# Kernel tuning notes

Hardware: AMD Instinct MI355X
Metric: run time of the kernel (lower is better)

The kernel has to match this reference:

```python
import jax, jax.numpy as jnp
import numpy as np
import math

N_HEAD = 16
HEAD_DIM = 64
BASE = 10000.0

def setup_inputs() -> dict:
    key = jax.random.key(0)
    k1, k2, k3, k4 = jax.random.split(key, 4)
    B, T, C = 2, 2048, 1024
    x = jax.random.normal(k1, (B, T, C), dtype=jnp.float32)
    w_attn = jax.random.normal(k2, (3 * C, C), dtype=jnp.float32) * 0.02
    w_proj = jax.random.normal(k3, (C, C), dtype=jnp.float32) * 0.02
    delta = jax.random.normal(k4, (N_HEAD, HEAD_DIM), dtype=jnp.float32) * 0.5
    return {"x": x, "w_attn": w_attn, "w_proj": w_proj, "delta": delta}

def reference(x, w_attn, w_proj, delta):
    B, T, C = x.shape
    H, D = N_HEAD, HEAD_DIM
    # qkv projection (nn.Linear, no bias): x @ W^T
    qkv = jnp.einsum('btc,ec->bte', x, w_attn)
    q, k, v = jnp.split(qkv, 3, axis=-1)
    q = q.reshape(B, T, H, D).transpose(0, 2, 1, 3)  # (B,H,T,D)
    k = k.reshape(B, T, H, D).transpose(0, 2, 1, 3)
    v = v.reshape(B, T, H, D).transpose(0, 2, 1, 3)
    # PoPE: d frequencies per head
    inv_freq = 1.0 / (BASE ** (jnp.arange(D, dtype=jnp.float32) / D))  # (D,)
    t = jnp.arange(T, dtype=jnp.float32)
    freqs = t[:, None] * inv_freq[None, :]            # (T,D)
    cos_pos = jnp.cos(freqs)[None, None]              # (1,1,T,D)
    sin_pos = jnp.sin(freqs)[None, None]
    mu_q = jax.nn.softplus(q)
    mu_k = jax.nn.softplus(k)
    d = jnp.clip(delta, -2.0 * math.pi, 0.0)          # (H,D)
    cos_d = jnp.cos(d)[None, :, None, :]              # (1,H,1,D)
    sin_d = jnp.sin(d)[None, :, None, :]
    q_real = mu_q * cos_pos
    q_imag = mu_q * sin_pos
    k_real = mu_k * (cos_pos * cos_d - sin_pos * sin_d)
    k_imag = mu_k * (sin_pos * cos_d + cos_pos * sin_d)
    scale = 1.0 / math.sqrt(D)
    att = (jnp.einsum('bhtd,bhsd->bhts', q_real, k_real)
           + jnp.einsum('bhtd,bhsd->bhts', q_imag, k_imag)) * scale
    causal = jnp.tril(jnp.ones((T, T), dtype=bool))
    att = jnp.where(causal[None, None], att, -jnp.inf)
    att = jax.nn.softmax(att, axis=-1)
    y = jnp.einsum('bhts,bhsd->bhtd', att, v)
    y = y.transpose(0, 2, 1, 3).reshape(B, T, C)
    return jnp.einsum('btc,ec->bte', y, w_proj)
```

## Files before the change

kernel.cpp:

```cpp
#include <hip/hip_runtime.h>
#include <math.h>

typedef short s16x8 __attribute__((ext_vector_type(8)));
typedef float f32x4 __attribute__((ext_vector_type(4)));
typedef float f32x16 __attribute__((ext_vector_type(16)));
typedef unsigned short u16;

#define B_ 2
#define T_ 2048
#define HN_ 16

__device__ __forceinline__ u16 f2bf(float f) {
  union { float f; unsigned u; } v; v.f = f;
  unsigned r = v.u + 0x7FFFu + ((v.u >> 16) & 1u);
  return (u16)(r >> 16);
}
__device__ __forceinline__ float bf2f(u16 b) {
  union { unsigned u; float f; } v; v.u = ((unsigned)b) << 16;
  return v.f;
}
__device__ __forceinline__ float softplus_f(float v) {
  return fmaxf(v, 0.f) + __logf(1.f + __expf(-fabsf(v)));
}
__device__ __forceinline__ f32x4 mfma16(s16x8 a, s16x8 b, f32x4 c) {
  return __builtin_amdgcn_mfma_f32_16x16x32_bf16(a, b, c, 0, 0, 0);
}
__device__ __forceinline__ f32x16 mfma32(s16x8 a, s16x8 b, f32x16 c) {
  return __builtin_amdgcn_mfma_f32_32x32x16_bf16(a, b, c, 0, 0, 0);
}
__device__ __forceinline__ void gload16(void* lds, const void* g) {
  __builtin_amdgcn_global_load_lds(
      (const __attribute__((address_space(1))) unsigned int*)g,
      (__attribute__((address_space(3))) unsigned int*)lds, 16, 0, 0);
}
__device__ __forceinline__ unsigned cvtpk(float lo, float hi) {
  unsigned r;
  asm("v_cvt_pk_bf16_f32 %0, %1, %2" : "=v"(r) : "v"(lo), "v"(hi));
  return r;
}

__device__ __constant__ unsigned char QTC[72][3] = {
  {15,0,64},{15,1,65},{15,2,66},{15,3,67},{15,4,68},{15,5,69},{15,6,70},{15,7,71},
  {14,0,56},{14,1,57},{14,2,58},{14,3,59},{14,4,60},{14,5,61},{14,6,62},{14,7,63},
  {13,0,49},{13,1,50},{13,2,51},{13,3,52},{13,4,53},{13,5,54},{13,6,55},
  {12,0,42},{12,1,43},{12,2,44},{12,3,45},{12,4,46},{12,5,47},{12,6,48},
  {11,0,36},{11,1,37},{11,2,38},{11,3,39},{11,4,40},{11,5,41},
  {10,0,30},{10,1,31},{10,2,32},{10,3,33},{10,4,34},{10,5,35},
  {9,0,25},{9,1,26},{9,2,27},{9,3,28},{9,4,29},
  {8,0,20},{8,1,21},{8,2,22},{8,3,23},{8,4,24},
  {7,0,16},{7,1,17},{7,2,18},{7,3,19},
  {6,0,12},{6,1,13},{6,2,14},{6,3,15},
  {5,0,9},{5,1,10},{5,2,11},
  {4,0,6},{4,1,7},{4,2,8},
  {3,0,4},{3,1,5},
  {2,0,2},{2,1,3},
  {1,0,1},
  {0,0,0}
};
__device__ __constant__ unsigned char OFFT[16] =
  {0,1,2,4,6,9,12,16,20,25,30,36,42,49,56,64};

__global__ __launch_bounds__(256) void conv_swz(
    const float* __restrict__ in, u16* __restrict__ out, int nchunks)
{
  int c = blockIdx.x * 256 + threadIdx.x;
  if (c >= nchunks) return;
  int row = c >> 7, cc = c & 127;
  int ks = cc >> 3, ch = cc & 7;
  const float4* src = (const float4*)(in + ((size_t)row << 10) + (cc << 3));
  float4 a = src[0], b = src[1];
  s16x8 o;
  o[0] = (short)f2bf(a.x); o[1] = (short)f2bf(a.y);
  o[2] = (short)f2bf(a.z); o[3] = (short)f2bf(a.w);
  o[4] = (short)f2bf(b.x); o[5] = (short)f2bf(b.y);
  o[6] = (short)f2bf(b.z); o[7] = (short)f2bf(b.w);
  *(s16x8*)(out + ((size_t)row << 10) + (ks << 6) + ((ch ^ (row & 7)) << 3)) = o;
}

__global__ __launch_bounds__(256) void build_tables(
    float* __restrict__ postab, float* __restrict__ dtab,
    const float* __restrict__ delta)
{
  int idx = blockIdx.x * 256 + threadIdx.x;
  int t = idx >> 6, d = idx & 63;
  float invf = powf(10000.f, -(float)d * (1.0f / 64.0f));
  float ang = (float)t * invf;
  float sp, cp;
  sincosf(ang, &sp, &cp);
  postab[idx * 2 + 0] = cp;
  postab[idx * 2 + 1] = sp;
  if (idx < HN_ * 64) {
    float dl = delta[idx];
    dl = fminf(fmaxf(dl, -6.2831853071795865f), 0.f);
    float sd, cd;
    sincosf(dl, &sd, &cd);
    dtab[idx * 2 + 0] = cd;
    dtab[idx * 2 + 1] = sd;
  }
}

template<int OUTK>
__global__ __launch_bounds__(256) void gemm_nt_mfma(
    const u16* __restrict__ A, const u16* __restrict__ Bw,
    void* __restrict__ Cout, int N)
{
  __shared__ u16 As[128 * 64];
  __shared__ u16 Bs[128 * 64];
  const int tid = threadIdx.x;
  const int w = tid >> 6, l = tid & 63, g = l >> 4;
  const int bm = blockIdx.y * 128, bn = blockIdx.x * 128;
  const int wr = w >> 1, wc = w & 1;
  const int K = 1024;

  const f32x4 zero = {0.f, 0.f, 0.f, 0.f};
  f32x4 acc[4][4];
  #pragma unroll
  for (int mt = 0; mt < 4; ++mt)
    #pragma unroll
    for (int nt = 0; nt < 4; ++nt) acc[mt][nt] = zero;

  for (int kt = 0; kt < K; kt += 64) {
    __syncthreads();
    #pragma unroll
    for (int j = 0; j < 4; ++j) {
      int cid = (j * 4 + w) * 64 + l;
      int row = cid >> 3, cc = cid & 7;
      gload16(As + ((j * 4 + w) << 9), A  + (size_t)(bm + row) * K + kt + cc * 8);
      gload16(Bs + ((j * 4 + w) << 9), Bw + (size_t)(bn + row) * K + kt + cc * 8);
    }
    __syncthreads();
    #pragma unroll
    for (int ks = 0; ks < 2; ++ks) {
      s16x8 af[4], bfr[4];
      #pragma unroll
      for (int mt = 0; mt < 4; ++mt) {
        int rr = wr * 64 + mt * 16 + (l & 15);
        af[mt] = *(const s16x8*)(As + rr * 64 + (((ks * 4 + g) ^ (rr & 7)) << 3));
      }
      #pragma unroll
      for (int nt = 0; nt < 4; ++nt) {
        int rr = wc * 64 + nt * 16 + (l & 15);
        bfr[nt] = *(const s16x8*)(Bs + rr * 64 + (((ks * 4 + g) ^ (rr & 7)) << 3));
      }
      #pragma unroll
      for (int mt = 0; mt < 4; ++mt)
        #pragma unroll
        for (int nt = 0; nt < 4; ++nt)
          acc[mt][nt] = mfma16(af[mt], bfr[nt], acc[mt][nt]);
    }
  }

  #pragma unroll
  for (int mt = 0; mt < 4; ++mt)
    #pragma unroll
    for (int nt = 0; nt < 4; ++nt)
      #pragma unroll
      for (int r = 0; r < 4; ++r) {
        int row = bm + wr * 64 + mt * 16 + g * 4 + r;
        int col = bn + wc * 64 + nt * 16 + (l & 15);
        if (OUTK == 0)
          ((u16*)Cout)[(size_t)row * N + col] = f2bf(acc[mt][nt][r]);
        else
          ((float*)Cout)[(size_t)row * N + col] = acc[mt][nt][r];
      }
}

__global__ __launch_bounds__(256) void pope_prep(
    const u16* __restrict__ qkvb, const float* __restrict__ postab,
    const float* __restrict__ dtab, u16* __restrict__ Kp, u16* __restrict__ Vtp,
    u16* __restrict__ Qp, float* __restrict__ qn, int* __restrict__ knmaxI)
{
  __shared__ u16 Vs[64][72];
  __shared__ float knsh[64];
  const int tb = blockIdx.x, h = blockIdx.y, b = blockIdx.z;
  const int t0 = tb * 64, tid = threadIdx.x;
  const int tl = tid >> 2, j = tid & 3, d0 = j * 16;
  const int t = t0 + tl;
  const size_t bh = (size_t)b * HN_ + h;
  const size_t qrow = (size_t)(b * T_ + t) * 3072 + h * 64;
  const float2* pt = (const float2*)postab + (size_t)t * 64 + d0;

  float kss = 0.f;
  {
    s16x8 k0 = *(const s16x8*)(qkvb + qrow + 1024 + d0);
    s16x8 k1 = *(const s16x8*)(qkvb + qrow + 1024 + d0 + 8);
    const float2* dt = (const float2*)dtab + h * 64 + d0;
    s16x8 r0, r1, i0, i1;
    #pragma unroll
    for (int i = 0; i < 8; ++i) {
      float mu = softplus_f(bf2f((u16)k0[i]));
      kss += mu * mu;
      float2 cs = pt[i]; float2 dc = dt[i];
      r0[i] = (short)f2bf(mu * (cs.x * dc.x - cs.y * dc.y));
      i0[i] = (short)f2bf(mu * (cs.y * dc.x + cs.x * dc.y));
    }
    #pragma unroll
    for (int i = 0; i < 8; ++i) {
      float mu = softplus_f(bf2f((u16)k1[i]));
      kss += mu * mu;
      float2 cs = pt[8 + i]; float2 dc = dt[8 + i];
      r1[i] = (short)f2bf(mu * (cs.x * dc.x - cs.y * dc.y));
      i1[i] = (short)f2bf(mu * (cs.y * dc.x + cs.x * dc.y));
    }
    u16* Krow = Kp + (bh * T_ + t) * 128;
    int sw = t & 7;
    int c0 = d0 >> 3;
    *(s16x8*)(Krow + ((c0 ^ sw) << 3))       = r0;
    *(s16x8*)(Krow + (((c0 + 1) ^ sw) << 3)) = r1;
    *(s16x8*)(Krow + (((c0 + 8) ^ sw) << 3)) = i0;
    *(s16x8*)(Krow + (((c0 + 9) ^ sw) << 3)) = i1;
  }
  kss += __shfl_xor(kss, 1);
  kss += __shfl_xor(kss, 2);
  if (j == 0) knsh[tl] = kss;

  float qss = 0.f;
  {
    s16x8 q0 = *(const s16x8*)(qkvb + qrow + d0);
    s16x8 q1 = *(const s16x8*)(qkvb + qrow + d0 + 8);
    s16x8 r0, r1, i0, i1;
    #pragma unroll
    for (int i = 0; i < 8; ++i) {
      float mu = softplus_f(bf2f((u16)q0[i]));
      qss += mu * mu;
      float2 cs = pt[i];
      r0[i] = (short)f2bf(mu * cs.x);
      i0[i] = (short)f2bf(mu * cs.y);
    }
    #pragma unroll
    for (int i = 0; i < 8; ++i) {
      float mu = softplus_f(bf2f((u16)q1[i]));
      qss += mu * mu;
      float2 cs = pt[8 + i];
      r1[i] = (short)f2bf(mu * cs.x);
      i1[i] = (short)f2bf(mu * cs.y);
    }
    u16* Qrow = Qp + (bh * T_ + t) * 128;
    *(s16x8*)(Qrow + d0)          = r0;
    *(s16x8*)(Qrow + d0 + 8)      = r1;
    *(s16x8*)(Qrow + 64 + d0)     = i0;
    *(s16x8*)(Qrow + 64 + d0 + 8) = i1;
  }
  qss += __shfl_xor(qss, 1);
  qss += __shfl_xor(qss, 2);
  if (j == 0) qn[bh * T_ + t] = sqrtf(qss);

  {
    s16x8 v0 = *(const s16x8*)(qkvb + qrow + 2048 + d0);
    s16x8 v1 = *(const s16x8*)(qkvb + qrow + 2048 + d0 + 8);
    *(s16x8*)(&Vs[tl][d0])     = v0;
    *(s16x8*)(&Vs[tl][d0 + 8]) = v1;
  }
  __syncthreads();
  if (tid == 0) {
    float mx = 0.f;
    #pragma unroll
    for (int i = 0; i < 64; ++i) mx = fmaxf(mx, knsh[i]);
    atomicMax(knmaxI + bh, __float_as_int(sqrtf(mx)));
  }
  {
    const int d = tid >> 2, jj = tid & 3, ts0 = jj * 16;
    u16* Vrow = Vtp + (bh * 64 + d) * T_;
    int swd = d & 7;
    s16x8 o0, o1;
    #pragma unroll
    for (int i = 0; i < 8; ++i) {
      o0[i] = (short)Vs[ts0 + i][d];
      o1[i] = (short)Vs[ts0 + 8 + i][d];
    }
    int cc0 = ts0 >> 3;
    *(s16x8*)(Vrow + t0 + ((cc0 ^ swd) << 3))       = o0;
    *(s16x8*)(Vrow + t0 + (((cc0 + 1) ^ swd) << 3)) = o1;
  }
}

__global__ __launch_bounds__(256) void attn_split(
    const u16* __restrict__ Qp, const u16* __restrict__ Kp,
    const u16* __restrict__ Vtp, const float* __restrict__ qn,
    const int* __restrict__ knmaxI, u16* __restrict__ po, float* __restrict__ pl)
{
  const int xcd = (int)blockIdx.x & 7;
  const int idx = (int)blockIdx.x >> 3;
  const int bh = xcd + 8 * (idx / 72);
  const int w72 = idx % 72;
  const int qt = QTC[w72][0], c = QTC[w72][1];
  const int slot = bh * 72 + QTC[w72][2];

  __shared__ u16 smem[2][12288];
  const int tid = threadIdx.x, w = tid >> 6, l = tid & 63;
  const int hi = l >> 5, ln = l & 31;

  const int kbeg = c * 256;
  const int kend0 = (qt + 1) * 128;
  const int kend = kend0 < kbeg + 256 ? kend0 : kbeg + 256;
  const int ntile = (kend - kbeg) >> 6;

  const float LS = 0.125f * 1.4426950408889634f;
  const u16* Kpb = Kp + (size_t)bh * T_ * 128;
  const u16* Vtb = Vtp + (size_t)bh * 64 * T_;

  auto STAGE = [&](int buf, int s0) {
    u16* Kd = smem[buf];
    u16* Vd = smem[buf] + 8192;
    #pragma unroll
    for (int jj = 0; jj < 4; ++jj) {
      int cid = (jj * 4 + w) * 64 + l;
      int row = cid >> 4, cc = cid & 15;
      gload16(Kd + ((jj * 4 + w) << 9), Kpb + (size_t)(s0 + row) * 128 + cc * 8);
    }
    #pragma unroll
    for (int jj = 0; jj < 2; ++jj) {
      int cid = (jj * 4 + w) * 64 + l;
      int row = cid >> 3, cc = cid & 7;
      gload16(Vd + ((jj * 4 + w) << 9), Vtb + (size_t)row * T_ + s0 + cc * 8);
    }
  };

  const int q = qt * 128 + w * 32 + ln;
  s16x8 qf[8];
  {
    const u16* qrp = Qp + ((size_t)bh * T_ + q) * 128;
    #pragma unroll
    for (int ks = 0; ks < 8; ++ks)
      qf[ks] = *(const s16x8*)(qrp + ks * 16 + hi * 8);
  }
  const float knm = __int_as_float(knmaxI[bh]);
  const float m = LS * qn[(size_t)bh * T_ + q] * knm;

  asm volatile("s_waitcnt vmcnt(0)" ::: "memory");

  const f32x16 zero16 = {0.f,0.f,0.f,0.f,0.f,0.f,0.f,0.f,
                         0.f,0.f,0.f,0.f,0.f,0.f,0.f,0.f};
  f32x16 o0 = zero16, o1 = zero16;
  float lsum = 0.f;
  const int qminw = qt * 128 + w * 32;

  STAGE(0, kbeg);
  int cur = 0;

  for (int ti = 0; ti < ntile; ++ti) {
    const int s0 = kbeg + ti * 64;
    if (ti + 1 < ntile) {
      STAGE(cur ^ 1, s0 + 64);
      asm volatile("s_waitcnt vmcnt(6)" ::: "memory");
    } else {
      asm volatile("s_waitcnt vmcnt(0)" ::: "memory");
    }
    __builtin_amdgcn_s_barrier();
    __builtin_amdgcn_sched_barrier(0);

    const u16* Ks  = smem[cur];
    const u16* Vts = smem[cur] + 8192;

    if (s0 <= qminw + 31) {
      const bool needmask = (s0 + 63) > qminw;

      f32x16 sacc0 = zero16, sacc1 = zero16;
      __builtin_amdgcn_s_setprio(1);
      #pragma unroll
      for (int ks = 0; ks < 8; ++ks) {
        int r0_ = ln, r1_ = 32 + ln;
        s16x8 kf0 = *(const s16x8*)(Ks + r0_ * 128 + (((2 * ks + hi) ^ (r0_ & 7)) << 3));
        s16x8 kf1 = *(const s16x8*)(Ks + r1_ * 128 + (((2 * ks + hi) ^ (r1_ & 7)) << 3));
        sacc0 = mfma32(kf0, qf[ks], sacc0);
        sacc1 = mfma32(kf1, qf[ks], sacc1);
      }
      __builtin_amdgcn_s_setprio(0);

      if (needmask) {
        #pragma unroll
        for (int jj = 0; jj < 16; ++jj) {
          int sg = s0 + (jj & 3) + 8 * (jj >> 2) + 4 * hi;
          if (sg > q)      sacc0[jj] = -3e38f;
          if (sg + 32 > q) sacc1[jj] = -3e38f;
        }
      }
      float rs = 0.f;
      #pragma unroll
      for (int jj = 0; jj < 16; ++jj) {
        float p0 = exp2f(fmaf(sacc0[jj], LS, -m));
        float p1 = exp2f(fmaf(sacc1[jj], LS, -m));
        sacc0[jj] = p0; sacc1[jj] = p1;
        rs += p0 + p1;
      }
      lsum += rs;

      s16x8 pa[4];
      #pragma unroll
      for (int ks = 0; ks < 4; ++ks) {
        const int bb = (ks & 1) * 8;
        unsigned a0, a1, b0v, b1v;
        if (ks < 2) {
          a0  = cvtpk(sacc0[bb + 0], sacc0[bb + 1]);
          a1  = cvtpk(sacc0[bb + 2], sacc0[bb + 3]);
          b0v = cvtpk(sacc0[bb + 4], sacc0[bb + 5]);
          b1v = cvtpk(sacc0[bb + 6], sacc0[bb + 7]);
        } else {
          a0  = cvtpk(sacc1[bb + 0], sacc1[bb + 1]);
          a1  = cvtpk(sacc1[bb + 2], sacc1[bb + 3]);
          b0v = cvtpk(sacc1[bb + 4], sacc1[bb + 5]);
          b1v = cvtpk(sacc1[bb + 6], sacc1[bb + 7]);
        }
        asm("v_permlane32_swap_b32 %0, %1" : "+v"(a0), "+v"(b0v));
        asm("v_permlane32_swap_b32 %0, %1" : "+v"(a1), "+v"(b1v));
        union { unsigned u[4]; s16x8 v; } pu;
        pu.u[0] = a0; pu.u[1] = a1; pu.u[2] = b0v; pu.u[3] = b1v;
        pa[ks] = pu.v;
      }

      __builtin_amdgcn_s_setprio(1);
      #pragma unroll
      for (int ks = 0; ks < 4; ++ks) {
        int rd0 = ln, rd1 = 32 + ln;
        s16x8 vb0 = *(const s16x8*)(Vts + rd0 * 64 + (((2 * ks + hi) ^ (rd0 & 7)) << 3));
        s16x8 vb1 = *(const s16x8*)(Vts + rd1 * 64 + (((2 * ks + hi) ^ (rd1 & 7)) << 3));
        o0 = mfma32(pa[ks], vb0, o0);
        o1 = mfma32(pa[ks], vb1, o1);
      }
      __builtin_amdgcn_s_setprio(0);
    }
    __builtin_amdgcn_s_barrier();
    cur ^= 1;
  }

  lsum += __shfl_xor(lsum, 32);
  u16* pob = po + (size_t)slot * 8192;
  #pragma unroll
  for (int jj = 0; jj < 16; ++jj) {
    int row = w * 32 + 4 * hi + (jj & 3) + 8 * (jj >> 2);
    pob[row * 64 + ln]      = f2bf(o0[jj]);
    pob[row * 64 + 32 + ln] = f2bf(o1[jj]);
  }
  if (hi == 0)
    pl[(size_t)slot * 128 + w * 32 + ln] = lsum;
}

__global__ __launch_bounds__(256) void attn_combine(
    const u16* __restrict__ po, const float* __restrict__ pl,
    u16* __restrict__ yb)
{
  const int xcd = (int)blockIdx.x & 7;
  const int i = (int)blockIdx.x >> 3;
  const int bh = xcd + 8 * (i & 3);
  const int qt = 15 - (i >> 2);
  const int b = bh >> 4, h = bh & 15;
  const int nch = (qt + 2) >> 1;
  const int base = bh * 72 + OFFT[qt];
  const int t = threadIdx.x;
  const int row = t >> 1, d0 = (t & 1) * 32;

  float acc[32];
  #pragma unroll
  for (int i2 = 0; i2 < 32; ++i2) acc[i2] = 0.f;
  float ls = 0.f;
  for (int c = 0; c < nch; ++c) {
    const u16* pr = po + (size_t)(base + c) * 8192 + row * 64 + d0;
    #pragma unroll
    for (int v = 0; v < 4; ++v) {
      s16x8 x = *(const s16x8*)(pr + v * 8);
      #pragma unroll
      for (int i2 = 0; i2 < 8; ++i2) acc[v * 8 + i2] += bf2f((u16)x[i2]);
    }
    ls += pl[(size_t)(base + c) * 128 + row];
  }
  float inv = 1.f / ls;
  int qrow = qt * 128 + row;
  size_t rb = (size_t)(b * T_ + qrow) * 1024 + h * 64;
  #pragma unroll
  for (int v = 0; v < 4; ++v) {
    int ch = ((d0 >> 3) + v) ^ (qrow & 7);
    s16x8 o;
    #pragma unroll
    for (int i2 = 0; i2 < 8; ++i2) o[i2] = (short)f2bf(acc[v * 8 + i2] * inv);
    *(s16x8*)(yb + rb + (ch << 3)) = o;
  }
}

extern "C" void kernel_launch(void* const* d_in, const int* in_sizes, int n_in,
                              void* d_out, int out_size, void* d_ws, size_t ws_size,
                              hipStream_t stream)
{
  const float* x      = (const float*)d_in[0];
  const float* w_attn = (const float*)d_in[1];
  const float* w_proj = (const float*)d_in[2];
  const float* delta  = (const float*)d_in[3];
  float* out = (float*)d_out;

  char* p = (char*)d_ws;
  u16* qkvb   = (u16*)p;
  u16* xb     = (u16*)(p + (size_t)4096 * 3072 * 2);
  u16* wab    = (u16*)(p + (size_t)4096 * 3072 * 2 + (size_t)4096 * 1024 * 2);
  u16* po     = (u16*)p;
  p += (size_t)(4096 * 3072 + 4096 * 1024 + 3072 * 1024) * 2;
  u16* wpb    = (u16*)p;  p += (size_t)1024 * 1024 * 2;
  u16* yb     = (u16*)p;  p += (size_t)4096 * 1024 * 2;
  u16* Kp     = (u16*)p;  p += (size_t)B_ * HN_ * T_ * 128 * 2;
  u16* Vtp    = (u16*)p;  p += (size_t)B_ * HN_ * 64 * T_ * 2;
  u16* Qp     = (u16*)p;  p += (size_t)B_ * HN_ * T_ * 128 * 2;
  float* postab = (float*)p; p += (size_t)T_ * 64 * 2 * 4;
  float* dtab   = (float*)p; p += (size_t)HN_ * 64 * 2 * 4;
  float* qn     = (float*)p; p += (size_t)B_ * HN_ * T_ * 4;
  float* pl     = (float*)p; p += (size_t)2304 * 128 * 4;
  int*   knmaxI = (int*)p;   p += 32 * 4;

  conv_swz<<<(4096 * 128) / 256, 256, 0, stream>>>(x, xb, 4096 * 128);
  conv_swz<<<(3072 * 128) / 256, 256, 0, stream>>>(w_attn, wab, 3072 * 128);
  conv_swz<<<(1024 * 128) / 256, 256, 0, stream>>>(w_proj, wpb, 1024 * 128);
  build_tables<<<(T_ * 64) / 256, 256, 0, stream>>>(postab, dtab, delta);
  hipMemsetAsync(knmaxI, 0, 32 * 4, stream);

  gemm_nt_mfma<0><<<dim3(3072 / 128, 4096 / 128), 256, 0, stream>>>(xb, wab, qkvb, 3072);
  pope_prep<<<dim3(T_ / 64, HN_, B_), 256, 0, stream>>>(qkvb, postab, dtab, Kp, Vtp,
                                                        Qp, qn, knmaxI);
  attn_split<<<dim3(2304), 256, 0, stream>>>(Qp, Kp, Vtp, qn, knmaxI, po, pl);
  attn_combine<<<dim3(512), 256, 0, stream>>>(po, pl, yb);
  gemm_nt_mfma<1><<<dim3(1024 / 128, 4096 / 128), 256, 0, stream>>>(yb, wpb, out, 1024);
}
```

Baseline: 163.8 us.

## Fuse PoPE prep into QKV GEMM epilogue and deepen attention K/V prefetch

The QKV GEMM epilogue now applies softplus and the PoPE rotation directly. It writes swizzled Qp/Kp, transposed V, the q norms and the per-head max k norm, so the bf16 qkv buffer and the separate pope_prep kernel are removed. The attention kernel issues the first two K/V tile stages before loading Q and restages a buffer after each tile's final barrier, which gives a deeper prefetch. The cost is a heavier GEMM epilogue that does scalar, less coalesced 2-byte stores plus transcendental math per element, and higher register pressure.

```diff
diff --git a/kernel.cpp b/kernel.cpp
--- a/kernel.cpp
+++ b/kernel.cpp
@@ -102,7 +102,10 @@
 template<int OUTK>
 __global__ __launch_bounds__(256) void gemm_nt_mfma(
     const u16* __restrict__ A, const u16* __restrict__ Bw,
-    void* __restrict__ Cout, int N)
+    void* __restrict__ Cout, int N,
+    const float* __restrict__ postab, const float* __restrict__ dtab,
+    u16* __restrict__ Qp, u16* __restrict__ Kp, u16* __restrict__ Vtp,
+    float* __restrict__ qn, int* __restrict__ knmaxI)
 {
   __shared__ u16 As[128 * 64];
   __shared__ u16 Bs[128 * 64];
@@ -150,127 +153,103 @@
     }
   }
 
-  #pragma unroll
-  for (int mt = 0; mt < 4; ++mt)
-    #pragma unroll
-    for (int nt = 0; nt < 4; ++nt)
-      #pragma unroll
-      for (int r = 0; r < 4; ++r) {
-        int row = bm + wr * 64 + mt * 16 + g * 4 + r;
-        int col = bn + wc * 64 + nt * 16 + (l & 15);
-        if (OUTK == 0)
-          ((u16*)Cout)[(size_t)row * N + col] = f2bf(acc[mt][nt][r]);
-        else
+  if (OUTK == 1) {
+    #pragma unroll
+    for (int mt = 0; mt < 4; ++mt)
+      #pragma unroll
+      for (int nt = 0; nt < 4; ++nt)
+        #pragma unroll
+        for (int r = 0; r < 4; ++r) {
+          int row = bm + wr * 64 + mt * 16 + g * 4 + r;
+          int col = bn + wc * 64 + nt * 16 + (l & 15);
           ((float*)Cout)[(size_t)row * N + col] = acc[mt][nt][r];
-      }
-}
-
-__global__ __launch_bounds__(256) void pope_prep(
-    const u16* __restrict__ qkvb, const float* __restrict__ postab,
-    const float* __restrict__ dtab, u16* __restrict__ Kp, u16* __restrict__ Vtp,
-    u16* __restrict__ Qp, float* __restrict__ qn, int* __restrict__ knmaxI)
-{
-  __shared__ u16 Vs[64][72];
-  __shared__ float knsh[64];
-  const int tb = blockIdx.x, h = blockIdx.y, b = blockIdx.z;
-  const int t0 = tb * 64, tid = threadIdx.x;
-  const int tl = tid >> 2, j = tid & 3, d0 = j * 16;
-  const int t = t0 + tl;
-  const size_t bh = (size_t)b * HN_ + h;
-  const size_t qrow = (size_t)(b * T_ + t) * 3072 + h * 64;
-  const float2* pt = (const float2*)postab + (size_t)t * 64 + d0;
-
-  float kss = 0.f;
-  {
-    s16x8 k0 = *(const s16x8*)(qkvb + qrow + 1024 + d0);
-    s16x8 k1 = *(const s16x8*)(qkvb + qrow + 1024 + d0 + 8);
-    const float2* dt = (const float2*)dtab + h * 64 + d0;
-    s16x8 r0, r1, i0, i1;
-    #pragma unroll
-    for (int i = 0; i < 8; ++i) {
-      float mu = softplus_f(bf2f((u16)k0[i]));
-      kss += mu * mu;
-      float2 cs = pt[i]; float2 dc = dt[i];
-      r0[i] = (short)f2bf(mu * (cs.x * dc.x - cs.y * dc.y));
-      i0[i] = (short)f2bf(mu * (cs.y * dc.x + cs.x * dc.y));
-    }
-    #pragma unroll
-    for (int i = 0; i < 8; ++i) {
-      float mu = softplus_f(bf2f((u16)k1[i]));
-      kss += mu * mu;
-      float2 cs = pt[8 + i]; float2 dc = dt[8 + i];
-      r1[i] = (short)f2bf(mu * (cs.x * dc.x - cs.y * dc.y));
-      i1[i] = (short)f2bf(mu * (cs.y * dc.x + cs.x * dc.y));
-    }
-    u16* Krow = Kp + (bh * T_ + t) * 128;
-    int sw = t & 7;
-    int c0 = d0 >> 3;
-    *(s16x8*)(Krow + ((c0 ^ sw) << 3))       = r0;
-    *(s16x8*)(Krow + (((c0 + 1) ^ sw) << 3)) = r1;
-    *(s16x8*)(Krow + (((c0 + 8) ^ sw) << 3)) = i0;
-    *(s16x8*)(Krow + (((c0 + 9) ^ sw) << 3)) = i1;
-  }
-  kss += __shfl_xor(kss, 1);
-  kss += __shfl_xor(kss, 2);
-  if (j == 0) knsh[tl] = kss;
-
-  float qss = 0.f;
-  {
-    s16x8 q0 = *(const s16x8*)(qkvb + qrow + d0);
-    s16x8 q1 = *(const s16x8*)(qkvb + qrow + d0 + 8);
-    s16x8 r0, r1, i0, i1;
-    #pragma unroll
-    for (int i = 0; i < 8; ++i) {
-      float mu = softplus_f(bf2f((u16)q0[i]));
-      qss += mu * mu;
-      float2 cs = pt[i];
-      r0[i] = (short)f2bf(mu * cs.x);
-      i0[i] = (short)f2bf(mu * cs.y);
-    }
-    #pragma unroll
-    for (int i = 0; i < 8; ++i) {
-      float mu = softplus_f(bf2f((u16)q1[i]));
-      qss += mu * mu;
-      float2 cs = pt[8 + i];
-      r1[i] = (short)f2bf(mu * cs.x);
-      i1[i] = (short)f2bf(mu * cs.y);
-    }
-    u16* Qrow = Qp + (bh * T_ + t) * 128;
-    *(s16x8*)(Qrow + d0)          = r0;
-    *(s16x8*)(Qrow + d0 + 8)      = r1;
-    *(s16x8*)(Qrow + 64 + d0)     = i0;
-    *(s16x8*)(Qrow + 64 + d0 + 8) = i1;
-  }
-  qss += __shfl_xor(qss, 1);
-  qss += __shfl_xor(qss, 2);
-  if (j == 0) qn[bh * T_ + t] = sqrtf(qss);
-
-  {
-    s16x8 v0 = *(const s16x8*)(qkvb + qrow + 2048 + d0);
-    s16x8 v1 = *(const s16x8*)(qkvb + qrow + 2048 + d0 + 8);
-    *(s16x8*)(&Vs[tl][d0])     = v0;
-    *(s16x8*)(&Vs[tl][d0 + 8]) = v1;
-  }
-  __syncthreads();
-  if (tid == 0) {
-    float mx = 0.f;
-    #pragma unroll
-    for (int i = 0; i < 64; ++i) mx = fmaxf(mx, knsh[i]);
-    atomicMax(knmaxI + bh, __float_as_int(sqrtf(mx)));
-  }
-  {
-    const int d = tid >> 2, jj = tid & 3, ts0 = jj * 16;
-    u16* Vrow = Vtp + (bh * 64 + d) * T_;
-    int swd = d & 7;
-    s16x8 o0, o1;
-    #pragma unroll
-    for (int i = 0; i < 8; ++i) {
-      o0[i] = (short)Vs[ts0 + i][d];
-      o1[i] = (short)Vs[ts0 + 8 + i][d];
-    }
-    int cc0 = ts0 >> 3;
-    *(s16x8*)(Vrow + t0 + ((cc0 ^ swd) << 3))       = o0;
-    *(s16x8*)(Vrow + t0 + (((cc0 + 1) ^ swd) << 3)) = o1;
+        }
+  } else {
+    const int third = bn >> 10;
+    const int h = ((bn & 1023) >> 6) + wc;
+    const int b = bm >> 11;
+    const size_t bhT = (size_t)(b * HN_ + h) * T_;
+
+    if (third == 2) {
+      #pragma unroll
+      for (int mt = 0; mt < 4; ++mt) {
+        const int t = (bm + wr * 64 + mt * 16 + g * 4) & 2047;
+        #pragma unroll
+        for (int nt = 0; nt < 4; ++nt) {
+          const int d = nt * 16 + (l & 15);
+          short4 sv;
+          sv.x = (short)f2bf(acc[mt][nt][0]);
+          sv.y = (short)f2bf(acc[mt][nt][1]);
+          sv.z = (short)f2bf(acc[mt][nt][2]);
+          sv.w = (short)f2bf(acc[mt][nt][3]);
+          const int ch = ((t & 63) >> 3) ^ (d & 7);
+          u16* dst = Vtp + ((size_t)(b * HN_ + h) * 64 + d) * T_
+                         + (t & ~63) + (ch << 3) + (t & 7);
+          *(short4*)dst = sv;
+        }
+      }
+    } else {
+      float rss[4][4];
+      #pragma unroll
+      for (int mt = 0; mt < 4; ++mt)
+        #pragma unroll
+        for (int r = 0; r < 4; ++r) rss[mt][r] = 0.f;
+
+      #pragma unroll
+      for (int mt = 0; mt < 4; ++mt)
+        #pragma unroll
+        for (int nt = 0; nt < 4; ++nt)
+          #pragma unroll
+          for (int r = 0; r < 4; ++r) {
+            const int t = (bm + wr * 64 + mt * 16 + g * 4 + r) & 2047;
+            const int d = nt * 16 + (l & 15);
+            float mu = softplus_f(acc[mt][nt][r]);
+            rss[mt][r] += mu * mu;
+            float2 cs = ((const float2*)postab)[t * 64 + d];
+            if (third == 0) {
+              Qp[(bhT + t) * 128 + d]      = f2bf(mu * cs.x);
+              Qp[(bhT + t) * 128 + 64 + d] = f2bf(mu * cs.y);
+            } else {
+              float2 dc = ((const float2*)dtab)[h * 64 + d];
+              const int sw = t & 7, c0 = d >> 3, dd = d & 7;
+              Kp[(bhT + t) * 128 + ((c0 ^ sw) << 3) + dd] =
+                  f2bf(mu * (cs.x * dc.x - cs.y * dc.y));
+              Kp[(bhT + t) * 128 + (((c0 + 8) ^ sw) << 3) + dd] =
+                  f2bf(mu * (cs.y * dc.x + cs.x * dc.y));
+            }
+          }
+      #pragma unroll
+      for (int mt = 0; mt < 4; ++mt)
+        #pragma unroll
+        for (int r = 0; r < 4; ++r) {
+          float s = rss[mt][r];
+          s += __shfl_xor(s, 1);
+          s += __shfl_xor(s, 2);
+          s += __shfl_xor(s, 4);
+          s += __shfl_xor(s, 8);
+          rss[mt][r] = s;
+        }
+      if (third == 0) {
+        if ((l & 15) == 0) {
+          #pragma unroll
+          for (int mt = 0; mt < 4; ++mt)
+            #pragma unroll
+            for (int r = 0; r < 4; ++r) {
+              const int t = (bm + wr * 64 + mt * 16 + g * 4 + r) & 2047;
+              qn[bhT + t] = sqrtf(rss[mt][r]);
+            }
+        }
+      } else {
+        float mx = 0.f;
+        #pragma unroll
+        for (int mt = 0; mt < 4; ++mt)
+          #pragma unroll
+          for (int r = 0; r < 4; ++r) mx = fmaxf(mx, rss[mt][r]);
+        mx = fmaxf(mx, __shfl_xor(mx, 16));
+        mx = fmaxf(mx, __shfl_xor(mx, 32));
+        if (l == 0) atomicMax(knmaxI + b * HN_ + h, __float_as_int(sqrtf(mx)));
+      }
+    }
   }
 }
 
@@ -316,6 +295,8 @@
     }
   };
 
+  STAGE(0, kbeg);
+
   const int q = qt * 128 + w * 32 + ln;
   s16x8 qf[8];
   {
@@ -327,7 +308,7 @@
   const float knm = __int_as_float(knmaxI[bh]);
   const float m = LS * qn[(size_t)bh * T_ + q] * knm;
 
-  asm volatile("s_waitcnt vmcnt(0)" ::: "memory");
+  STAGE(1, kbeg + 64);
 
   const f32x16 zero16 = {0.f,0.f,0.f,0.f,0.f,0.f,0.f,0.f,
                          0.f,0.f,0.f,0.f,0.f,0.f,0.f,0.f};
@@ -335,22 +316,17 @@
   float lsum = 0.f;
   const int qminw = qt * 128 + w * 32;
 
-  STAGE(0, kbeg);
-  int cur = 0;
-
   for (int ti = 0; ti < ntile; ++ti) {
     const int s0 = kbeg + ti * 64;
-    if (ti + 1 < ntile) {
-      STAGE(cur ^ 1, s0 + 64);
+    if (ti + 1 < ntile)
       asm volatile("s_waitcnt vmcnt(6)" ::: "memory");
-    } else {
+    else
       asm volatile("s_waitcnt vmcnt(0)" ::: "memory");
-    }
     __builtin_amdgcn_s_barrier();
     __builtin_amdgcn_sched_barrier(0);
 
-    const u16* Ks  = smem[cur];
-    const u16* Vts = smem[cur] + 8192;
+    const u16* Ks  = smem[ti & 1];
+    const u16* Vts = smem[ti & 1] + 8192;
 
     if (s0 <= qminw + 31) {
       const bool needmask = (s0 + 63) > qminw;
@@ -420,7 +396,7 @@
       __builtin_amdgcn_s_setprio(0);
     }
     __builtin_amdgcn_s_barrier();
-    cur ^= 1;
+    if (ti + 2 < ntile) STAGE(ti & 1, s0 + 128);
   }
 
   lsum += __shfl_xor(lsum, 32);
@@ -487,7 +463,6 @@
   float* out = (float*)d_out;
 
   char* p = (char*)d_ws;
-  u16* qkvb   = (u16*)p;
   u16* xb     = (u16*)(p + (size_t)4096 * 3072 * 2);
   u16* wab    = (u16*)(p + (size_t)4096 * 3072 * 2 + (size_t)4096 * 1024 * 2);
   u16* po     = (u16*)p;
@@ -509,10 +484,10 @@
   build_tables<<<(T_ * 64) / 256, 256, 0, stream>>>(postab, dtab, delta);
   hipMemsetAsync(knmaxI, 0, 32 * 4, stream);
 
-  gemm_nt_mfma<0><<<dim3(3072 / 128, 4096 / 128), 256, 0, stream>>>(xb, wab, qkvb, 3072);
-  pope_prep<<<dim3(T_ / 64, HN_, B_), 256, 0, stream>>>(qkvb, postab, dtab, Kp, Vtp,
-                                                        Qp, qn, knmaxI);
+  gemm_nt_mfma<2><<<dim3(3072 / 128, 4096 / 128), 256, 0, stream>>>(
+      xb, wab, nullptr, 3072, postab, dtab, Qp, Kp, Vtp, qn, knmaxI);
   attn_split<<<dim3(2304), 256, 0, stream>>>(Qp, Kp, Vtp, qn, knmaxI, po, pl);
   attn_combine<<<dim3(512), 256, 0, stream>>>(po, pl, yb);
-  gemm_nt_mfma<1><<<dim3(1024 / 128, 4096 / 128), 256, 0, stream>>>(yb, wpb, out, 1024);
-}
+  gemm_nt_mfma<1><<<dim3(1024 / 128, 4096 / 128), 256, 0, stream>>>(
+      yb, wpb, out, 1024, nullptr, nullptr, nullptr, nullptr, nullptr, nullptr, nullptr);
+}
```

Result: slower. 224.4 us (+37.0%).
